# Kernel tuning notes

Hardware: AMD Instinct MI355X
Metric: run time of the kernel (lower is better)

## Reference

```python
import jax, jax.numpy as jnp
import numpy as np

N_HEADS = 16

def _rope_tables(L, head_dim, dtype):
    inv_freq = 1.0 / (10000.0 ** (jnp.arange(0, head_dim, 2, dtype=jnp.float32) / head_dim))
    t = jnp.arange(L, dtype=jnp.float32)
    freqs = jnp.outer(t, inv_freq)            # [L, head_dim/2]
    emb = jnp.concatenate([freqs, freqs], -1)  # [L, head_dim]
    return jnp.cos(emb).astype(dtype), jnp.sin(emb).astype(dtype)

def _apply_rope(x, cos, sin):
    # x: [B, L, H, hd]; cos/sin: [1, L, 1, hd]
    half = x.shape[-1] // 2
    x1, x2 = x[..., :half], x[..., half:]
    x_rot = jnp.concatenate([-x2, x1], -1)
    return x * cos + x_rot * sin

def setup_inputs() -> dict:
    key = jax.random.key(0)
    ks = jax.random.split(key, 5)
    D = 1024
    s = 0.02
    return {
        "x": jax.random.normal(ks[0], (4, 2048, D), jnp.float32),
        "w_qkv": jax.random.normal(ks[1], (3 * D, D), jnp.float32) * s,
        "b_qkv": jax.random.normal(ks[2], (3 * D,), jnp.float32) * s,
        "w_out": jax.random.normal(ks[3], (D, D), jnp.float32) * s,
        "b_out": jax.random.normal(ks[4], (D,), jnp.float32) * s,
    }

def reference(x, w_qkv, b_qkv, w_out, b_out):
    B, L, D = x.shape
    H = N_HEADS
    hd = D // H
    scale = hd ** -0.5
    qkv = (x @ w_qkv.T + b_qkv).reshape(B, L, 3, H, hd)
    q, k, v = qkv[:, :, 0], qkv[:, :, 1], qkv[:, :, 2]  # [B,L,H,hd]
    cos, sin = _rope_tables(L, hd, x.dtype)
    cos = cos[None, :, None, :]
    sin = sin[None, :, None, :]
    q = _apply_rope(q, cos, sin)
    k = _apply_rope(k, cos, sin)
    # [B,H,L,L] scores, non-causal softmax
    attn = jnp.einsum('blhd,bmhd->bhlm', q, k) * scale
    attn = jax.nn.softmax(attn, axis=-1)
    out = jnp.einsum('bhlm,bmhd->blhd', attn, v).reshape(B, L, D)
    return out @ w_out.T + b_out
```

## Files before the change

### kernel.cpp

```cpp
#include <hip/hip_runtime.h>
#include <stdint.h>

typedef __attribute__((ext_vector_type(4))) float f32x4;
typedef __attribute__((ext_vector_type(8))) short bf16x8;
typedef __attribute__((ext_vector_type(4))) short s16x4;
typedef __attribute__((ext_vector_type(4))) float fp32x4;

#define QSCALE 0.18033688f

__device__ __forceinline__ short f2bf(float f) {
    union { float f; unsigned u; } v; v.f = f;
    unsigned u = v.u;
    unsigned r = u + 0x7fffu + ((u >> 16) & 1u);
    return (short)(r >> 16);
}
__device__ __forceinline__ unsigned cvtpk(float a, float b) {
    unsigned r;
    asm("v_cvt_pk_bf16_f32 %0, %1, %2" : "=v"(r) : "v"(a), "v"(b));
    return r;
}

__device__ __forceinline__ void gld_lds16(const void* g, void* l) {
    __builtin_amdgcn_global_load_lds(
        (const __attribute__((address_space(1))) unsigned int*)(uintptr_t)g,
        (__attribute__((address_space(3))) unsigned int*)(uintptr_t)l,
        16, 0, 0);
}

__global__ __launch_bounds__(256) void prep_kernel(const float* __restrict__ x,
                                                   const float* __restrict__ wq,
                                                   const float* __restrict__ wo,
                                                   short* __restrict__ xb,
                                                   short* __restrict__ wqb,
                                                   short* __restrict__ wob,
                                                   float* __restrict__ tab) {
    int bid = blockIdx.x, tid = threadIdx.x;
    if (bid < 6144) {
        const float* in; short* out; int base;
        if (bid < 4096)      { in = x;  out = xb;  base = bid; }
        else if (bid < 5632) { in = wq; out = wqb; base = bid - 4096; }
        else                 { in = wo; out = wob; base = bid - 5632; }
        int idx = (base * 256 + tid) * 8;
        fp32x4 a = *(const fp32x4*)&in[idx];
        fp32x4 b = *(const fp32x4*)&in[idx + 4];
        union { unsigned w[4]; bf16x8 v; } u;
        u.w[0] = cvtpk(a[0], a[1]); u.w[1] = cvtpk(a[2], a[3]);
        u.w[2] = cvtpk(b[0], b[1]); u.w[3] = cvtpk(b[2], b[3]);
        *(bf16x8*)&out[idx] = u.v;
    } else {
        int idx = (bid - 6144) * 256 + tid;
        int l = idx >> 5, d = idx & 31;
        float inv = expf(-(float)d / 32.f * logf(10000.f));
        float ang = (float)l * inv;
        tab[idx * 2 + 0] = cosf(ang);
        tab[idx * 2 + 1] = sinf(ang);
    }
}

template<int MODE>
__global__ __launch_bounds__(256, 4)
void gemm_bt(const short* __restrict__ A,
             const short* __restrict__ B,
             const float* __restrict__ bias,
             void* __restrict__ Cout,
             short* __restrict__ VTout,
             const float* __restrict__ tab,
             int M, int N, int K) {
    __shared__ short lds[2 * 8192];
    const int tid = threadIdx.x;
    const int lane = tid & 63, wave = tid >> 6;
    const int i15 = lane & 15, g = lane >> 4;
    const int wr = wave >> 1, wc = wave & 1;

    const int nbx = gridDim.x;
    int bid = blockIdx.y * nbx + blockIdx.x;
    const int xcd = bid & 7, idx = bid >> 3;
    const int nchunk = nbx >> 3;
    const int n0 = (xcd * nchunk + (idx % nchunk)) * 128;
    const int m0 = (idx / nchunk) * 128;

    const int csw = (g ^ (i15 & 3)) * 8;
    const int aoff = (wr * 64 + i15) * 32 + csw;
    const int boff = (wc * 64 + i15) * 32 + csw;

    const int sr = lane >> 2;
    const int sc = ((lane & 3) ^ (sr & 3)) * 8;
    const short* a0 = A + (size_t)(m0 + (0 * 4 + wave) * 16 + sr) * K + sc;
    const short* a1 = A + (size_t)(m0 + (1 * 4 + wave) * 16 + sr) * K + sc;
    const short* b0 = B + (size_t)(n0 + (0 * 4 + wave) * 16 + sr) * K + sc;
    const short* b1 = B + (size_t)(n0 + (1 * 4 + wave) * 16 + sr) * K + sc;

#define STAGE(slot)                                                  \
    do {                                                             \
        gld_lds16(a0, lds + (slot) * 8192 + (0 * 4 + wave) * 512);   \
        gld_lds16(a1, lds + (slot) * 8192 + (1 * 4 + wave) * 512);   \
        gld_lds16(b0, lds + (slot) * 8192 + 4096 + (0 * 4 + wave) * 512); \
        gld_lds16(b1, lds + (slot) * 8192 + 4096 + (1 * 4 + wave) * 512); \
        a0 += 32; a1 += 32; b0 += 32; b1 += 32;                      \
    } while (0)

    STAGE(0);

    f32x4 acc[4][4] = {};
    const int NT = K >> 5;

    for (int T = 0; T < NT; ++T) {
        const int cur = T & 1;
        if (T > 0) {
            __builtin_amdgcn_s_barrier();
            __builtin_amdgcn_sched_barrier(0);
        }
        if (T + 1 < NT) {
            STAGE(cur ^ 1);
            asm volatile("s_waitcnt vmcnt(4)" ::: "memory");
        } else {
            asm volatile("s_waitcnt vmcnt(0)" ::: "memory");
        }
        __builtin_amdgcn_s_barrier();
        __builtin_amdgcn_sched_barrier(0);

        const short* As_ = lds + cur * 8192;
        const short* Bs_ = As_ + 4096;
        bf16x8 af[4], bfr[4];
#pragma unroll
        for (int m = 0; m < 4; ++m) af[m] = *(const bf16x8*)&As_[aoff + m * 512];
#pragma unroll
        for (int n = 0; n < 4; ++n) bfr[n] = *(const bf16x8*)&Bs_[boff + n * 512];
        __builtin_amdgcn_s_setprio(1);
#pragma unroll
        for (int m = 0; m < 4; ++m)
#pragma unroll
            for (int n = 0; n < 4; ++n)
                acc[m][n] = __builtin_amdgcn_mfma_f32_16x16x32_bf16(af[m], bfr[n], acc[m][n], 0, 0, 0);
        __builtin_amdgcn_s_setprio(0);
    }
#undef STAGE

    if (MODE == 0) {
#pragma unroll
        for (int m = 0; m < 4; ++m)
#pragma unroll
            for (int n = 0; n < 4; ++n) {
                int col = n0 + wc * 64 + n * 16 + i15;
                float bcol = bias[col];
#pragma unroll
                for (int j = 0; j < 4; ++j) {
                    int row = m0 + wr * 64 + m * 16 + g * 4 + j;
                    ((float*)Cout)[(size_t)row * N + col] = acc[m][n][j] + bcol;
                }
            }
    } else {
        const int sec = n0 >> 10;
        if (sec < 2) {
            const float qs = (sec == 0) ? QSCALE : 1.0f;
            short* out = (short*)Cout;
#pragma unroll
            for (int m = 0; m < 4; ++m) {
#pragma unroll
                for (int pp = 0; pp < 2; ++pp) {
                    int d = pp * 16 + i15;
                    int collo = n0 + wc * 64 + pp * 16 + i15;
                    float blo = bias[collo], bhi = bias[collo + 32];
#pragma unroll
                    for (int j = 0; j < 4; ++j) {
                        int row = m0 + wr * 64 + m * 16 + g * 4 + j;
                        int l = row & 2047;
                        float2 cs = *(const float2*)&tab[(l * 32 + d) * 2];
                        float x1 = acc[m][pp][j] + blo;
                        float x2 = acc[m][pp + 2][j] + bhi;
                        out[(size_t)row * 3072 + collo]      = f2bf((x1 * cs.x - x2 * cs.y) * qs);
                        out[(size_t)row * 3072 + collo + 32] = f2bf((x2 * cs.x + x1 * cs.y) * qs);
                    }
                }
            }
        } else {
#pragma unroll
            for (int m = 0; m < 4; ++m) {
                int rbase = m0 + wr * 64 + m * 16 + g * 4;
                int lbase = rbase & 2047, bidx = rbase >> 11;
#pragma unroll
                for (int n = 0; n < 4; ++n) {
                    int vcol = (n0 - 2048) + wc * 64 + n * 16 + i15;
                    int h = vcol >> 6, d = vcol & 63;
                    float bb = bias[n0 + wc * 64 + n * 16 + i15];
                    union { unsigned w[2]; s16x4 v; } u;
                    u.w[0] = cvtpk(acc[m][n][0] + bb, acc[m][n][1] + bb);
                    u.w[1] = cvtpk(acc[m][n][2] + bb, acc[m][n][3] + bb);
                    *(s16x4*)&VTout[((size_t)(bidx * 16 + h) * 64 + d) * 2048 + lbase] = u.v;
                }
            }
        }
    }
}

__global__ __launch_bounds__(256, 4) void attn_kernel(const short* __restrict__ qkv,
                                                      const short* __restrict__ VT,
                                                      short* __restrict__ O) {
    __shared__ short Ks[2][64 * 64];
    __shared__ short Vs[2][64 * 64];
    int orig = blockIdx.x;
    int xcd = orig & 7, idx = orig >> 3;
    int bh = xcd * 8 + (idx >> 4), qt = idx & 15;
    int b = bh >> 4, h = bh & 15;
    int tid = threadIdx.x, lane = tid & 63, wave = tid >> 6;
    int i15 = lane & 15, g = lane >> 4;
    int q0 = qt * 128;

    size_t qbase = (size_t)(b * 2048 + q0 + wave * 32);
    bf16x8 qf[2][2];
#pragma unroll
    for (int qg = 0; qg < 2; ++qg) {
        qf[qg][0] = *(const bf16x8*)&qkv[(qbase + qg * 16 + i15) * 3072 + h * 64 + 0  + g * 8];
        qf[qg][1] = *(const bf16x8*)&qkv[(qbase + qg * 16 + i15) * 3072 + h * 64 + 32 + g * 8];
    }

    bf16x8 onesf;
#pragma unroll
    for (int e = 0; e < 8; ++e) onesf[e] = (short)0x3F80;

    const int srow = tid >> 3;
    const int ss8 = (tid & 7) ^ (srow & 7);
    const int pr0 = (srow & 0x23) | ((srow & 0x10) >> 2) | ((srow & 0x0C) << 1);
    const int sr1 = srow + 32;
    const int pr1 = (sr1 & 0x23) | ((sr1 & 0x10) >> 2) | ((sr1 & 0x0C) << 1);
    const short* kb_ = qkv + (size_t)(b * 2048) * 3072 + 1024 + h * 64 + ss8 * 8;
    const short* kp0 = kb_ + (size_t)pr0 * 3072;
    const short* kp1 = kb_ + (size_t)pr1 * 3072;
    const short* vb_ = VT + (size_t)bh * 64 * 2048 + ss8 * 8;
    const short* vp0 = vb_ + (size_t)srow * 2048;
    const short* vp1 = vb_ + (size_t)sr1 * 2048;

    const int xr3 = i15 & 3, xb2 = (i15 >> 2) & 1;
    const int cLo = g ^ xr3;
    const int o0 = i15 * 64 + (xb2 * 4 + cLo) * 8;
    const int o1 = i15 * 64 + ((1 ^ xb2) * 4 + cLo) * 8;

    f32x4 acc_o[2][4] = {};
    f32x4 acc_l[2] = {};

#define STAGE(bk, bv)                                        \
    do {                                                     \
        gld_lds16(kp0, (bk) + wave * 512);                   \
        gld_lds16(kp1, (bk) + 2048 + wave * 512);            \
        gld_lds16(vp0, (bv) + wave * 512);                   \
        gld_lds16(vp1, (bv) + 2048 + wave * 512);            \
        kp0 += (size_t)64 * 3072; kp1 += (size_t)64 * 3072;  \
        vp0 += 64; vp1 += 64;                                \
    } while (0)

    STAGE(Ks[0], Vs[0]);

    for (int t = 0; t < 32; ++t) {
        const int cur = t & 1;
        if (t > 0) {
            __builtin_amdgcn_s_barrier();
            __builtin_amdgcn_sched_barrier(0);
        }
        if (t + 1 < 32) {
            STAGE(Ks[cur ^ 1], Vs[cur ^ 1]);
            asm volatile("s_waitcnt vmcnt(4)" ::: "memory");
        } else {
            asm volatile("s_waitcnt vmcnt(0)" ::: "memory");
        }
        __builtin_amdgcn_s_barrier();
        __builtin_amdgcn_sched_barrier(0);

        const short* ks = Ks[cur];
        const short* vs = Vs[cur];

        f32x4 sa[2][4] = {};
        __builtin_amdgcn_s_setprio(1);
#pragma unroll
        for (int kb = 0; kb < 2; ++kb) {
            const int ko = kb ? o1 : o0;
            bf16x8 kf[4];
#pragma unroll
            for (int jb = 0; jb < 4; ++jb) kf[jb] = *(const bf16x8*)&ks[ko + jb * 1024];
#pragma unroll
            for (int qg = 0; qg < 2; ++qg)
#pragma unroll
                for (int jb = 0; jb < 4; ++jb)
                    sa[qg][jb] = __builtin_amdgcn_mfma_f32_16x16x32_bf16(kf[jb], qf[qg][kb], sa[qg][jb], 0, 0, 0);
        }
        __builtin_amdgcn_s_setprio(0);

        bf16x8 pf[2][2];
#pragma unroll
        for (int qg = 0; qg < 2; ++qg) {
            float p[4][4];
#pragma unroll
            for (int jb = 0; jb < 4; ++jb)
#pragma unroll
                for (int r = 0; r < 4; ++r)
                    p[jb][r] = __builtin_amdgcn_exp2f(sa[qg][jb][r]);
#pragma unroll
            for (int kb = 0; kb < 2; ++kb) {
                union { unsigned w[4]; bf16x8 v; } u;
                u.w[0] = cvtpk(p[2 * kb][0],     p[2 * kb][1]);
                u.w[1] = cvtpk(p[2 * kb][2],     p[2 * kb][3]);
                u.w[2] = cvtpk(p[2 * kb + 1][0], p[2 * kb + 1][1]);
                u.w[3] = cvtpk(p[2 * kb + 1][2], p[2 * kb + 1][3]);
                pf[qg][kb] = u.v;
            }
        }

        __builtin_amdgcn_s_setprio(1);
#pragma unroll
        for (int db = 0; db < 4; ++db) {
#pragma unroll
            for (int kb = 0; kb < 2; ++kb) {
                bf16x8 vf = *(const bf16x8*)&vs[(kb ? o1 : o0) + db * 1024];
#pragma unroll
                for (int qg = 0; qg < 2; ++qg)
                    acc_o[qg][db] = __builtin_amdgcn_mfma_f32_16x16x32_bf16(pf[qg][kb], vf, acc_o[qg][db], 0, 0, 0);
            }
        }
#pragma unroll
        for (int qg = 0; qg < 2; ++qg) {
            acc_l[qg] = __builtin_amdgcn_mfma_f32_16x16x32_bf16(pf[qg][0], onesf, acc_l[qg], 0, 0, 0);
            acc_l[qg] = __builtin_amdgcn_mfma_f32_16x16x32_bf16(pf[qg][1], onesf, acc_l[qg], 0, 0, 0);
        }
        __builtin_amdgcn_s_setprio(0);
    }
#undef STAGE

#pragma unroll
    for (int qg = 0; qg < 2; ++qg) {
        float linv4[4];
#pragma unroll
        for (int r = 0; r < 4; ++r) linv4[r] = 1.f / acc_l[qg][r];
#pragma unroll
        for (int db = 0; db < 4; ++db) {
            int ocol = h * 64 + db * 16 + i15;
#pragma unroll
            for (int r = 0; r < 4; ++r) {
                size_t orow = qbase + qg * 16 + g * 4 + r;
                O[orow * 1024 + ocol] = f2bf(acc_o[qg][db][r] * linv4[r]);
            }
        }
    }
}

extern "C" void kernel_launch(void* const* d_in, const int* in_sizes, int n_in,
                              void* d_out, int out_size, void* d_ws, size_t ws_size,
                              hipStream_t stream) {
    const float* x     = (const float*)d_in[0];
    const float* w_qkv = (const float*)d_in[1];
    const float* b_qkv = (const float*)d_in[2];
    const float* w_out = (const float*)d_in[3];
    const float* b_out = (const float*)d_in[4];

    char* ws = (char*)d_ws;
    short* qkvb = (short*)(ws);
    short* xb   = (short*)(ws + 50331648);
    short* wqb  = (short*)(ws + 67108864);
    short* wob  = (short*)(ws + 73400320);
    short* VT   = (short*)(ws + 75497472);
    float* rt   = (float*)(ws + 92274688);
    short* Ob   = xb;

    prep_kernel<<<6400, 256, 0, stream>>>(x, w_qkv, w_out, xb, wqb, wob, rt);

    gemm_bt<1><<<dim3(24, 64), 256, 0, stream>>>(xb, wqb, b_qkv, qkvb, VT, rt, 8192, 3072, 1024);
    attn_kernel<<<1024, 256, 0, stream>>>(qkvb, VT, Ob);
    gemm_bt<0><<<dim3(8, 64), 256, 0, stream>>>(Ob, wob, b_out, d_out, nullptr, nullptr, 8192, 1024, 1024);
}
```

Baseline: 174.6 us.

## Re-swizzle GEMM LDS tile layout and raise occupancy hint to five blocks

Replaces the per-wave 16-row staging layout of the bf16 GEMM with a different XOR swizzle: each thread loads two rows' worth of 8-element chunks, and the MFMA fragment read offsets are recomputed to match. The aim is to cut LDS bank conflicts on fragment reads and to make the global loads more contiguous. The launch-bounds minimum blocks per CU goes from 4 to 5, which limits registers per thread and may cause spills. The LDS destination expression passes a per-lane address to a wave-uniform load-to-LDS intrinsic, so correctness depends on how the compiler handles that.

```diff
diff --git a/kernel.cpp b/kernel.cpp
--- a/kernel.cpp
+++ b/kernel.cpp
@@ -58,7 +58,7 @@
 }
 
 template<int MODE>
-__global__ __launch_bounds__(256, 4)
+__global__ __launch_bounds__(256, 5)
 void gemm_bt(const short* __restrict__ A,
              const short* __restrict__ B,
              const float* __restrict__ bias,
@@ -79,24 +79,26 @@
     const int n0 = (xcd * nchunk + (idx % nchunk)) * 128;
     const int m0 = (idx / nchunk) * 128;
 
-    const int csw = (g ^ (i15 & 3)) * 8;
-    const int aoff = (wr * 64 + i15) * 32 + csw;
-    const int boff = (wc * 64 + i15) * 32 + csw;
-
-    const int sr = lane >> 2;
-    const int sc = ((lane & 3) ^ (sr & 3)) * 8;
-    const short* a0 = A + (size_t)(m0 + (0 * 4 + wave) * 16 + sr) * K + sc;
-    const short* a1 = A + (size_t)(m0 + (1 * 4 + wave) * 16 + sr) * K + sc;
-    const short* b0 = B + (size_t)(n0 + (0 * 4 + wave) * 16 + sr) * K + sc;
-    const short* b1 = B + (size_t)(n0 + (1 * 4 + wave) * 16 + sr) * K + sc;
-
-#define STAGE(slot)                                                  \
-    do {                                                             \
-        gld_lds16(a0, lds + (slot) * 8192 + (0 * 4 + wave) * 512);   \
-        gld_lds16(a1, lds + (slot) * 8192 + (1 * 4 + wave) * 512);   \
-        gld_lds16(b0, lds + (slot) * 8192 + 4096 + (0 * 4 + wave) * 512); \
-        gld_lds16(b1, lds + (slot) * 8192 + 4096 + (1 * 4 + wave) * 512); \
-        a0 += 32; a1 += 32; b0 += 32; b1 += 32;                      \
+    const int pb = i15 >> 1;
+    const int sr = (((i15 & 1) << 2) | g) ^ pb;
+    const int aoff = (wr * 32 + pb) * 64 + sr * 8;
+    const int boff = (wc * 32 + pb) * 64 + sr * 8;
+
+    const int s0 = (tid & 7) ^ ((tid >> 3) & 7);
+    const int row0 = 2 * (tid >> 3) + (s0 >> 2);
+    const int kc = (s0 & 3) * 8;
+    const short* pA0 = A + (size_t)(m0 + row0) * K + kc;
+    const short* pA1 = A + (size_t)(m0 + row0 + 64) * K + kc;
+    const short* pB0 = B + (size_t)(n0 + row0) * K + kc;
+    const short* pB1 = B + (size_t)(n0 + row0 + 64) * K + kc;
+
+#define STAGE(slot)                                                   \
+    do {                                                              \
+        gld_lds16(pA0, lds + (slot) * 8192 + 0 * 2048 + tid * 8 - (lane * 8) + (lane * 8)); \
+        gld_lds16(pA1, lds + (slot) * 8192 + 1 * 2048 + tid * 8 - (lane * 8) + (lane * 8)); \
+        gld_lds16(pB0, lds + (slot) * 8192 + 4096 + 0 * 2048 + tid * 8 - (lane * 8) + (lane * 8)); \
+        gld_lds16(pB1, lds + (slot) * 8192 + 4096 + 1 * 2048 + tid * 8 - (lane * 8) + (lane * 8)); \
+        pA0 += 32; pA1 += 32; pB0 += 32; pB1 += 32;                   \
     } while (0)
 
     STAGE(0);
```

Measured after the change: 400.0 us. 2.29x slower.
